# Kernel tuning notes

Hardware: AMD Instinct MI355X
Metric: run time of the kernel (lower is better)

## Reference

```python
import jax, jax.numpy as jnp
import numpy as np

B, C, HEADS, D, DKQ = 1024, 512, 8, 64, 8
DV = C // HEADS                 # 64, dim_head_v
QKVC = DV + 2 * DKQ             # 80, qkv channels per head
EPS = 1e-5


def _bn(x, g, b, m, v):
    # eval-mode batchnorm, channel axis = 1
    shp = (1, -1) + (1,) * (x.ndim - 2)
    scale = g.reshape(shp) / jnp.sqrt(v.reshape(shp) + EPS)
    return (x - m.reshape(shp)) * scale + b.reshape(shp)


def _rel_index():
    i = np.arange(D)
    # key_index - query_index + D - 1, row-major flatten -> (D*D,)
    return jnp.asarray((i[:, None] - i[None, :] + D - 1).reshape(-1))


def setup_inputs() -> dict:
    key = jax.random.key(0)
    ks = jax.random.split(key, 16)
    O = HEADS * QKVC
    d = {
        "x": jax.random.normal(ks[0], (B, C, D), jnp.float32),
        "conv_w": jax.random.normal(ks[1], (O, C), jnp.float32) * 0.02,
        "bn1_g": jax.random.normal(ks[2], (O,), jnp.float32) * 0.1 + 1.0,
        "bn1_b": jax.random.normal(ks[3], (O,), jnp.float32) * 0.1,
        "bn1_m": jax.random.normal(ks[4], (O,), jnp.float32) * 0.1,
        "bn1_v": jax.random.uniform(ks[5], (O,), jnp.float32) * 0.5 + 0.5,
        "rel": jax.random.normal(ks[6], (QKVC, 2 * D - 1), jnp.float32),
        "bn2_g": jax.random.normal(ks[7], (3 * HEADS,), jnp.float32) * 0.1 + 1.0,
        "bn2_b": jax.random.normal(ks[8], (3 * HEADS,), jnp.float32) * 0.1,
        "bn2_m": jax.random.normal(ks[9], (3 * HEADS,), jnp.float32) * 0.1,
        "bn2_v": jax.random.uniform(ks[10], (3 * HEADS,), jnp.float32) * 0.5 + 0.5,
        "bn3_g": jax.random.normal(ks[11], (2 * C,), jnp.float32) * 0.1 + 1.0,
        "bn3_b": jax.random.normal(ks[12], (2 * C,), jnp.float32) * 0.1,
        "bn3_m": jax.random.normal(ks[13], (2 * C,), jnp.float32) * 0.1,
        "bn3_v": jax.random.uniform(ks[14], (2 * C,), jnp.float32) * 0.5 + 0.5,
    }
    return d


def reference(x, conv_w, bn1_g, bn1_b, bn1_m, bn1_v, rel,
              bn2_g, bn2_b, bn2_m, bn2_v, bn3_g, bn3_b, bn3_m, bn3_v):
    # 1x1 conv1d + BN1d: [B, O, D]
    qkv = jnp.einsum('oc,bcd->bod', conv_w, x)
    qkv = _bn(qkv, bn1_g, bn1_b, bn1_m, bn1_v)
    # rearrange 'b (q h) d -> b h q d' with q=QKVC, h=HEADS (channel = q*H + h)
    qkv = qkv.reshape(B, QKVC, HEADS, D).transpose(0, 2, 1, 3)  # [B,H,QKVC,D]
    q = qkv[:, :, :DKQ]                # [B,H,DKQ,D]
    k = qkv[:, :, DKQ:2 * DKQ]         # [B,H,DKQ,D]
    v = qkv[:, :, 2 * DKQ:]            # [B,H,DV,D]

    # relative positional embeddings gathered from table
    emb = rel[:, _rel_index()].reshape(QKVC, D, D)
    r_q, r_k, r_v = emb[:DKQ], emb[DKQ:2 * DKQ], emb[2 * DKQ:]

    qr = jnp.einsum('bhid,idj->bhdj', q, r_q)
    kr = jnp.einsum('bhid,idj->bhdj', k, r_k)
    dots = jnp.einsum('bhid,bhij->bhdj', q, k)

    # rearrange 'n b h d j -> b (h n) d j'  (channel = h*3 + n)
    stacked = jnp.stack([qr, kr, dots], axis=2).reshape(B, 3 * HEADS, D, D)
    stacked = _bn(stacked, bn2_g, bn2_b, bn2_m, bn2_v)
    norm_dots = stacked.reshape(B, HEADS, 3, D, D).sum(axis=2)  # [B,H,D,D]

    attn = jax.nn.softmax(norm_dots, axis=-1)
    out = jnp.einsum('bhdj,bhij->bhid', attn, v)      # [B,H,DV,D]
    kv = jnp.einsum('bhdj,idj->bhid', attn, r_v)      # [B,H,DV,D]

    # rearrange 'n b h i d -> b (n h i) d'  (channel = n*H*DV + h*DV + i)
    st = jnp.stack([kv, out], axis=1).reshape(B, 2 * HEADS * DV, D)
    st = _bn(st, bn3_g, bn3_b, bn3_m, bn3_v)
    return st.reshape(B, 2, HEADS * DV, D).sum(axis=1)  # [B,C,D]
```

## Files before the change

### kernel.cpp

```cpp
#include <hip/hip_runtime.h>
#include <hip/hip_bf16.h>

#define B_    1024
#define C_    512
#define H_    8
#define D_    64
#define EPS_  1e-5f

typedef __attribute__((ext_vector_type(4))) float f32x4;
typedef __attribute__((ext_vector_type(8))) short bf16x8;
typedef __attribute__((ext_vector_type(8))) unsigned short u16x8;

__device__ __forceinline__ float bf2f(unsigned short h) {
    union { unsigned int u; float f; } c;
    c.u = ((unsigned int)h) << 16;
    return c.f;
}
__device__ __forceinline__ unsigned short f2bf(float f) {
    __hip_bfloat16 h = __float2bfloat16(f);
    return *reinterpret_cast<unsigned short*>(&h);
}

__global__ __launch_bounds__(256) void k0_wconv(
    const float* __restrict__ w, unsigned short* __restrict__ wf)
{
    int t = blockIdx.x * 256 + threadIdx.x;
    int o  = t >> 6;
    int c0 = (t & 63) * 8;
    const float* src = w + (size_t)o * C_ + c0;
    u16x8 p;
#pragma unroll
    for (int e = 0; e < 8; ++e) p[e] = f2bf(src[e]);
    int f = (o >> 4) * 16 + (c0 >> 5);
    int l = (o & 15) | (((c0 >> 3) & 3) << 4);
    *reinterpret_cast<u16x8*>(&wf[(size_t)f * 512 + l * 8]) = p;
}

__global__ __launch_bounds__(256) void k0_tables(
    const float* __restrict__ rel,
    const float* __restrict__ g2, const float* __restrict__ v2,
    const float* __restrict__ g3, const float* __restrict__ v3,
    unsigned short* __restrict__ relB, unsigned short* __restrict__ relvA)
{
    int tid = blockIdx.x * 256 + threadIdx.x;
    if (tid < 4096) {
        int h = tid >> 9, uf = (tid >> 6) & 7, l = tid & 63;
        int u = uf * 16 + (l & 15);
        int g = l >> 4;
        float sq = g2[3*h]     * rsqrtf(v2[3*h]     + EPS_);
        float sk = g2[3*h + 1] * rsqrtf(v2[3*h + 1] + EPS_);
        u16x8 p;
#pragma unroll
        for (int e = 0; e < 8; ++e) {
            int s = g * 8 + e;
            float val = 0.f;
            if (u < 127 && s < 16)
                val = (s < 8 ? sq : sk) * rel[s * 127 + u];
            p[e] = f2bf(val);
        }
        *reinterpret_cast<u16x8*>(&relB[(size_t)tid * 8]) = p;
    } else if (tid < 4096 + 8192) {
        int t2 = tid - 4096;
        int h = t2 >> 10, iF = (t2 >> 8) & 3, tt = (t2 >> 6) & 3, l = t2 & 63;
        int i = iF * 16 + (l & 15);
        int c3 = h * 64 + i;
        float scl = g3[c3] * rsqrtf(v3[c3] + EPS_);
        const float* rrow = rel + (size_t)(16 + i) * 127;
        u16x8 p;
#pragma unroll
        for (int e = 0; e < 8; ++e) {
            int u = (l >> 4) * 8 + e + 32 * tt;
            p[e] = f2bf((u < 127) ? scl * rrow[u] : 0.f);
        }
        *reinterpret_cast<u16x8*>(&relvA[(size_t)t2 * 8]) = p;
    }
}

#define LDW1 72

__global__ __launch_bounds__(512) void k1_gemm(
    const float* __restrict__ x, const unsigned short* __restrict__ wf,
    const float* __restrict__ g1, const float* __restrict__ b1,
    const float* __restrict__ m1, const float* __restrict__ v1,
    const float* __restrict__ g3, const float* __restrict__ v3,
    unsigned short* __restrict__ qkA, unsigned short* __restrict__ vB)
{
    __shared__ unsigned short xt[2][64 * LDW1];
    __shared__ float ssc[640], ssh[640];

    const int tid = threadIdx.x;
    const int b   = blockIdx.x;

    for (int t = tid; t < 640; t += 512) {
        float sc = g1[t] * rsqrtf(v1[t] + EPS_);
        float sh = b1[t] - m1[t] * sc;
        int cc = t >> 3, hh = t & 7;
        if (cc >= 16) {
            int c3 = 512 + hh * 64 + (cc - 16);
            float f = g3[c3] * rsqrtf(v3[c3] + EPS_);
            sc *= f; sh *= f;
        }
        ssc[t] = sc;
        ssh[t] = sh;
    }

    const int lane = tid & 63;
    const int wv   = tid >> 6;
    const int lm   = lane & 15;
    const int lg   = lane >> 4;

    const float* xb = x + (size_t)b * C_ * D_;
    const int cp = tid >> 4;
    const int c4 = (tid & 15) * 4;

    f32x4 acc[5][4];
#pragma unroll
    for (int i = 0; i < 5; ++i)
#pragma unroll
        for (int j = 0; j < 4; ++j) acc[i][j] = (f32x4){0.f, 0.f, 0.f, 0.f};

    {
        f32x4 a = *reinterpret_cast<const f32x4*>(&xb[(2 * cp) * 64 + c4]);
        f32x4 c = *reinterpret_cast<const f32x4*>(&xb[(2 * cp + 1) * 64 + c4]);
#pragma unroll
        for (int j = 0; j < 4; ++j) {
            unsigned int pk = (unsigned int)f2bf(a[j]) | ((unsigned int)f2bf(c[j]) << 16);
            *reinterpret_cast<unsigned int*>(&xt[0][(c4 + j) * LDW1 + 2 * cp]) = pk;
        }
    }
    __syncthreads();

    int cur = 0;
    for (int kt = 0; kt < 8; ++kt) {
        f32x4 pa, pc;
        if (kt < 7) {
            pa = *reinterpret_cast<const f32x4*>(&xb[((kt + 1) * 64 + 2 * cp) * 64 + c4]);
            pc = *reinterpret_cast<const f32x4*>(&xb[((kt + 1) * 64 + 2 * cp + 1) * 64 + c4]);
        }
#pragma unroll
        for (int ks = 0; ks < 2; ++ks) {
            bf16x8 af[5];
#pragma unroll
            for (int fm = 0; fm < 5; ++fm) {
                size_t f = (size_t)((wv * 5 + fm) * 16 + kt * 2 + ks) * 512;
                af[fm] = *reinterpret_cast<const bf16x8*>(&wf[f + lane * 8]);
            }
            bf16x8 bfr[4];
#pragma unroll
            for (int fn = 0; fn < 4; ++fn)
                bfr[fn] = *reinterpret_cast<const bf16x8*>(
                    &xt[cur][(fn * 16 + lm) * LDW1 + ks * 32 + lg * 8]);
#pragma unroll
            for (int fm = 0; fm < 5; ++fm)
#pragma unroll
                for (int fn = 0; fn < 4; ++fn)
                    acc[fm][fn] = __builtin_amdgcn_mfma_f32_16x16x32_bf16(
                        af[fm], bfr[fn], acc[fm][fn], 0, 0, 0);
        }
        if (kt < 7) {
#pragma unroll
            for (int j = 0; j < 4; ++j) {
                unsigned int pk = (unsigned int)f2bf(pa[j]) | ((unsigned int)f2bf(pc[j]) << 16);
                *reinterpret_cast<unsigned int*>(&xt[cur ^ 1][(c4 + j) * LDW1 + 2 * cp]) = pk;
            }
        }
        __syncthreads();
        cur ^= 1;
    }

#pragma unroll
    for (int fm = 0; fm < 5; ++fm) {
#pragma unroll
        for (int fn = 0; fn < 4; ++fn) {
            int d = fn * 16 + lm;
#pragma unroll
            for (int r = 0; r < 4; ++r) {
                int o = wv * 80 + fm * 16 + lg * 4 + r;
                int cc = o >> 3, hh = o & 7;
                float val = acc[fm][fn][r] * ssc[o] + ssh[o];
                unsigned short bv = f2bf(val);
                if (cc < 8)
                    qkA[(((size_t)b * 8 + hh) * 4 + (d >> 4)) * 512 + (d & 15) * 8 + cc] = bv;
                else if (cc < 16)
                    qkA[(((size_t)b * 8 + hh) * 4 + (d >> 4)) * 512 + ((d & 15) + 16) * 8 + (cc - 8)] = bv;
                else
                    vB[((size_t)(b * 8 + hh) * 64 + (cc - 16)) * 64 + d] = bv;
            }
        }
    }
    for (int z = tid; z < 4096; z += 512) {
        int hh  = z >> 9;
        int mf  = (z >> 7) & 3;
        int off = z & 127;
        unsigned int* p = reinterpret_cast<unsigned int*>(
            qkA + (((size_t)b * 8 + hh) * 4 + mf) * 512 + 256);
        p[off] = 0u;
    }
}

#define SGP 84
#define SA  72
#define RLD 136

__global__ __launch_bounds__(256) void k2_attn(
    const unsigned short* __restrict__ qkA, const unsigned short* __restrict__ vB,
    const unsigned short* __restrict__ relB, const unsigned short* __restrict__ relvA,
    const float* __restrict__ g2, const float* __restrict__ v2,
    const float* __restrict__ g3, const float* __restrict__ b3,
    const float* __restrict__ m3, const float* __restrict__ v3,
    float* __restrict__ outp)
{
    __shared__ float          SGb[64 * SGP];
    __shared__ unsigned short attn[64 * SA];
    __shared__ unsigned short A2[64 * RLD];
    __shared__ float sh3[64];

    const int tid  = threadIdx.x;
    const int b    = blockIdx.x >> 3;
    const int h    = blockIdx.x & 7;
    const int lane = tid & 63;
    const int w    = tid >> 6;
    const int lmm  = lane & 15;
    const int lg   = lane >> 4;

    const unsigned short* qbase = qkA + ((size_t)(b * 8 + h) * 4) * 512;

    for (int i = tid; i < 64 * RLD / 2; i += 256)
        reinterpret_cast<unsigned int*>(A2)[i] = 0u;
    if (tid < 64) {
        int c = h * 64 + tid;
        float sa = g3[c] * rsqrtf(v3[c] + EPS_);
        float sb = g3[512 + c] * rsqrtf(v3[512 + c] + EPS_);
        sh3[tid] = (b3[c] - m3[c] * sa) + (b3[512 + c] - m3[512 + c] * sb);
    }
    const float s_dt = g2[3 * h + 2] * rsqrtf(v2[3 * h + 2] + EPS_);

    bf16x8 aA = *reinterpret_cast<const bf16x8*>(&qbase[w * 512 + lane * 8]);
    bf16x8 zv = {0, 0, 0, 0, 0, 0, 0, 0};
    bf16x8 kBf[4];
#pragma unroll
    for (int jf = 0; jf < 4; ++jf) {
        kBf[jf] = zv;
        if (lane < 16)
            kBf[jf] = *reinterpret_cast<const bf16x8*>(&qbase[jf * 512 + (lane + 16) * 8]);
    }
    bf16x8 rBf[8];
#pragma unroll
    for (int uf = 0; uf < 8; ++uf)
        rBf[uf] = *reinterpret_cast<const bf16x8*>(&relB[(size_t)(h * 8 + uf) * 512 + lane * 8]);

    f32x4 dotsAcc[4];
#pragma unroll
    for (int jf = 0; jf < 4; ++jf)
        dotsAcc[jf] = __builtin_amdgcn_mfma_f32_16x16x32_bf16(
            aA, kBf[jf], (f32x4){0.f, 0.f, 0.f, 0.f}, 0, 0, 0);
    f32x4 sgAcc[8];
#pragma unroll
    for (int uf = 0; uf < 8; ++uf)
        sgAcc[uf] = __builtin_amdgcn_mfma_f32_16x16x32_bf16(
            aA, rBf[uf], (f32x4){0.f, 0.f, 0.f, 0.f}, 0, 0, 0);

#pragma unroll
    for (int uf = 0; uf < 8; ++uf) {
#pragma unroll
        for (int r = 0; r < 4; ++r) {
            int d = (w << 4) + (lg << 2) + r;
            int t = uf * 16 + lmm - d + 15;
            if (t >= 0 && t < 79)
                SGb[d * SGP + t] = sgAcc[uf][r];
        }
    }
    __syncthreads();

#pragma unroll
    for (int r = 0; r < 4; ++r) {
        int d = (w << 4) + (lg << 2) + r;
        const float* sgr = &SGb[d * SGP];
        float sc0 = s_dt * dotsAcc[0][r] + sgr[78 - lmm];
        float sc1 = s_dt * dotsAcc[1][r] + sgr[62 - lmm];
        float sc2 = s_dt * dotsAcc[2][r] + sgr[46 - lmm];
        float sc3 = s_dt * dotsAcc[3][r] + sgr[30 - lmm];
        float mx = fmaxf(fmaxf(sc0, sc1), fmaxf(sc2, sc3));
        mx = fmaxf(mx, __shfl_xor(mx, 1));
        mx = fmaxf(mx, __shfl_xor(mx, 2));
        mx = fmaxf(mx, __shfl_xor(mx, 4));
        mx = fmaxf(mx, __shfl_xor(mx, 8));
        float e0 = __expf(sc0 - mx), e1 = __expf(sc1 - mx);
        float e2 = __expf(sc2 - mx), e3 = __expf(sc3 - mx);
        float sum = (e0 + e1) + (e2 + e3);
        sum += __shfl_xor(sum, 1);
        sum += __shfl_xor(sum, 2);
        sum += __shfl_xor(sum, 4);
        sum += __shfl_xor(sum, 8);
        float inv = 1.f / sum;
        unsigned short p0 = f2bf(e0 * inv), p1 = f2bf(e1 * inv);
        unsigned short p2 = f2bf(e2 * inv), p3 = f2bf(e3 * inv);
        attn[d * SA + lmm]      = p0;
        attn[d * SA + 16 + lmm] = p1;
        attn[d * SA + 32 + lmm] = p2;
        attn[d * SA + 48 + lmm] = p3;
        A2[d * RLD + 63 + d - lmm] = p0;
        A2[d * RLD + 47 + d - lmm] = p1;
        A2[d * RLD + 31 + d - lmm] = p2;
        A2[d * RLD + 15 + d - lmm] = p3;
    }

    const int lk8  = lg * 8;
    const int irow = (w << 4) + lmm;
    const unsigned short* vbase = vB + (size_t)(b * 8 + h) * 4096;
    bf16x8 av0 = *reinterpret_cast<const bf16x8*>(&vbase[irow * 64 + lk8]);
    bf16x8 av1 = *reinterpret_cast<const bf16x8*>(&vbase[irow * 64 + 32 + lk8]);
    bf16x8 rvA[4];
#pragma unroll
    for (int t = 0; t < 4; ++t)
        rvA[t] = *reinterpret_cast<const bf16x8*>(
            &relvA[(size_t)(((h * 4 + w) * 4 + t)) * 512 + lane * 8]);

    __syncthreads();

    f32x4 acc[4];
#pragma unroll
    for (int nf = 0; nf < 4; ++nf) acc[nf] = (f32x4){0.f, 0.f, 0.f, 0.f};

#pragma unroll
    for (int nf = 0; nf < 4; ++nf) {
        const unsigned short* arow = &attn[(nf * 16 + lmm) * SA + lk8];
        acc[nf] = __builtin_amdgcn_mfma_f32_16x16x32_bf16(
            av0, *reinterpret_cast<const bf16x8*>(&arow[0]), acc[nf], 0, 0, 0);
        acc[nf] = __builtin_amdgcn_mfma_f32_16x16x32_bf16(
            av1, *reinterpret_cast<const bf16x8*>(&arow[32]), acc[nf], 0, 0, 0);
        const unsigned short* a2row = &A2[(nf * 16 + lmm) * RLD + lk8];
        acc[nf] = __builtin_amdgcn_mfma_f32_16x16x32_bf16(
            rvA[0], *reinterpret_cast<const bf16x8*>(&a2row[0]), acc[nf], 0, 0, 0);
        acc[nf] = __builtin_amdgcn_mfma_f32_16x16x32_bf16(
            rvA[1], *reinterpret_cast<const bf16x8*>(&a2row[32]), acc[nf], 0, 0, 0);
        acc[nf] = __builtin_amdgcn_mfma_f32_16x16x32_bf16(
            rvA[2], *reinterpret_cast<const bf16x8*>(&a2row[64]), acc[nf], 0, 0, 0);
        acc[nf] = __builtin_amdgcn_mfma_f32_16x16x32_bf16(
            rvA[3], *reinterpret_cast<const bf16x8*>(&a2row[96]), acc[nf], 0, 0, 0);
    }

    float* op = outp + ((size_t)b * 512 + h * 64) * 64;
    const int r0 = lg * 4;
#pragma unroll
    for (int r = 0; r < 4; ++r) {
        int i = (w << 4) + r0 + r;
        float sh = sh3[i];
#pragma unroll
        for (int nf = 0; nf < 4; ++nf)
            op[(size_t)i * 64 + nf * 16 + lmm] = acc[nf][r] + sh;
    }
}

extern "C" void kernel_launch(void* const* d_in, const int* in_sizes, int n_in,
                              void* d_out, int out_size, void* d_ws, size_t ws_size,
                              hipStream_t stream) {
    (void)in_sizes; (void)n_in; (void)out_size; (void)ws_size;
    const float* x   = (const float*)d_in[0];
    const float* w   = (const float*)d_in[1];
    const float* g1  = (const float*)d_in[2];
    const float* b1  = (const float*)d_in[3];
    const float* m1  = (const float*)d_in[4];
    const float* v1  = (const float*)d_in[5];
    const float* rel = (const float*)d_in[6];
    const float* g2  = (const float*)d_in[7];
    const float* b2  = (const float*)d_in[8];  (void)b2;
    const float* m2  = (const float*)d_in[9];  (void)m2;
    const float* v2  = (const float*)d_in[10];
    const float* g3  = (const float*)d_in[11];
    const float* b3  = (const float*)d_in[12];
    const float* m3  = (const float*)d_in[13];
    const float* v3  = (const float*)d_in[14];
    float* out = (float*)d_out;

    unsigned short* wfrag = (unsigned short*)d_ws;
    unsigned short* relB  = (unsigned short*)((char*)d_ws + 655360);
    unsigned short* relvA = (unsigned short*)((char*)d_ws + 720896);
    unsigned short* qkA   = (unsigned short*)((char*)d_ws + 1048576);
    unsigned short* vB    = (unsigned short*)((char*)d_ws + 1048576 + (size_t)33554432);

    hipLaunchKernelGGL(k0_wconv, dim3(160), dim3(256), 0, stream, w, wfrag);
    hipLaunchKernelGGL(k0_tables, dim3(48), dim3(256), 0, stream,
                       rel, g2, v2, g3, v3, relB, relvA);
    hipLaunchKernelGGL(k1_gemm, dim3(1024), dim3(512), 0, stream,
                       x, wfrag, g1, b1, m1, v1, g3, v3, qkA, vB);
    hipLaunchKernelGGL(k2_attn, dim3(8192), dim3(256), 0, stream,
                       qkA, vB, relB, relvA, g2, v2, g3, b3, m3, v3, out);
}
```

Before: 192.1 us.

## Stage whole x tile into fragment-ordered LDS once instead of double-buffered k-loop

The QKV projection GEMM now loads the full 512x64 x slice for a batch element into shared memory in one up-front pass. It stores it in MFMA B-fragment order, so each lane reads a contiguous 16-byte vector with no padding. The previous double-buffered loop, with a barrier per k-tile, is replaced by a fully unrolled 16-step MFMA loop with no intermediate syncs. A launch-bounds occupancy hint is also added. The costs are 64KB of LDS per block, which limits blocks per CU, and no overlap between the global loads and the MFMAs.

New measurement: 207.8 us. 8.2% more time.

```diff
diff --git a/kernel.cpp b/kernel.cpp
--- a/kernel.cpp
+++ b/kernel.cpp
@@ -76,16 +76,14 @@
     }
 }
 
-#define LDW1 72
-
-__global__ __launch_bounds__(512) void k1_gemm(
+__global__ __launch_bounds__(512, 4) void k1_gemm(
     const float* __restrict__ x, const unsigned short* __restrict__ wf,
     const float* __restrict__ g1, const float* __restrict__ b1,
     const float* __restrict__ m1, const float* __restrict__ v1,
     const float* __restrict__ g3, const float* __restrict__ v3,
     unsigned short* __restrict__ qkA, unsigned short* __restrict__ vB)
 {
-    __shared__ unsigned short xt[2][64 * LDW1];
+    __shared__ unsigned short xf[16 * 4 * 64 * 8];
     __shared__ float ssc[640], ssh[640];
 
     const int tid = threadIdx.x;
@@ -104,68 +102,60 @@
         ssh[t] = sh;
     }
 
+    const float* xb = x + (size_t)b * C_ * D_;
+#pragma unroll
+    for (int it = 0; it < 2; ++it) {
+        int t  = tid + it * 512;
+        int c0 = (t >> 4) * 8;
+        int d0 = (t & 15) * 4;
+        f32x4 row[8];
+#pragma unroll
+        for (int cc = 0; cc < 8; ++cc)
+            row[cc] = *reinterpret_cast<const f32x4*>(&xb[(c0 + cc) * 64 + d0]);
+        int ks = c0 >> 5;
+        int kg = (c0 >> 3) & 3;
+#pragma unroll
+        for (int dd = 0; dd < 4; ++dd) {
+            int d  = d0 + dd;
+            int fn = d >> 4;
+            int ln = (d & 15) | (kg << 4);
+            u16x8 p;
+#pragma unroll
+            for (int e = 0; e < 8; ++e) p[e] = f2bf(row[e][dd]);
+            *reinterpret_cast<u16x8*>(&xf[((ks * 4 + fn) * 64 + ln) * 8]) = p;
+        }
+    }
+    __syncthreads();
+
     const int lane = tid & 63;
     const int wv   = tid >> 6;
     const int lm   = lane & 15;
     const int lg   = lane >> 4;
 
-    const float* xb = x + (size_t)b * C_ * D_;
-    const int cp = tid >> 4;
-    const int c4 = (tid & 15) * 4;
-
     f32x4 acc[5][4];
 #pragma unroll
     for (int i = 0; i < 5; ++i)
 #pragma unroll
         for (int j = 0; j < 4; ++j) acc[i][j] = (f32x4){0.f, 0.f, 0.f, 0.f};
 
-    {
-        f32x4 a = *reinterpret_cast<const f32x4*>(&xb[(2 * cp) * 64 + c4]);
-        f32x4 c = *reinterpret_cast<const f32x4*>(&xb[(2 * cp + 1) * 64 + c4]);
-#pragma unroll
-        for (int j = 0; j < 4; ++j) {
-            unsigned int pk = (unsigned int)f2bf(a[j]) | ((unsigned int)f2bf(c[j]) << 16);
-            *reinterpret_cast<unsigned int*>(&xt[0][(c4 + j) * LDW1 + 2 * cp]) = pk;
-        }
-    }
-    __syncthreads();
-
-    int cur = 0;
-    for (int kt = 0; kt < 8; ++kt) {
-        f32x4 pa, pc;
-        if (kt < 7) {
-            pa = *reinterpret_cast<const f32x4*>(&xb[((kt + 1) * 64 + 2 * cp) * 64 + c4]);
-            pc = *reinterpret_cast<const f32x4*>(&xb[((kt + 1) * 64 + 2 * cp + 1) * 64 + c4]);
-        }
-#pragma unroll
-        for (int ks = 0; ks < 2; ++ks) {
-            bf16x8 af[5];
-#pragma unroll
-            for (int fm = 0; fm < 5; ++fm) {
-                size_t f = (size_t)((wv * 5 + fm) * 16 + kt * 2 + ks) * 512;
-                af[fm] = *reinterpret_cast<const bf16x8*>(&wf[f + lane * 8]);
-            }
-            bf16x8 bfr[4];
+    const unsigned short* wfw = wf + (size_t)(wv * 5) * 16 * 512 + lane * 8;
+    const unsigned short* xfl = xf + lane * 8;
+
+#pragma unroll
+    for (int ks = 0; ks < 16; ++ks) {
+        bf16x8 af[5], bfr[4];
+#pragma unroll
+        for (int fm = 0; fm < 5; ++fm)
+            af[fm] = *reinterpret_cast<const bf16x8*>(&wfw[(size_t)(fm * 16 + ks) * 512]);
+#pragma unroll
+        for (int fn = 0; fn < 4; ++fn)
+            bfr[fn] = *reinterpret_cast<const bf16x8*>(&xfl[(ks * 4 + fn) * 512]);
+#pragma unroll
+        for (int fm = 0; fm < 5; ++fm)
 #pragma unroll
             for (int fn = 0; fn < 4; ++fn)
-                bfr[fn] = *reinterpret_cast<const bf16x8*>(
-                    &xt[cur][(fn * 16 + lm) * LDW1 + ks * 32 + lg * 8]);
-#pragma unroll
-            for (int fm = 0; fm < 5; ++fm)
-#pragma unroll
-                for (int fn = 0; fn < 4; ++fn)
-                    acc[fm][fn] = __builtin_amdgcn_mfma_f32_16x16x32_bf16(
-                        af[fm], bfr[fn], acc[fm][fn], 0, 0, 0);
-        }
-        if (kt < 7) {
-#pragma unroll
-            for (int j = 0; j < 4; ++j) {
-                unsigned int pk = (unsigned int)f2bf(pa[j]) | ((unsigned int)f2bf(pc[j]) << 16);
-                *reinterpret_cast<unsigned int*>(&xt[cur ^ 1][(c4 + j) * LDW1 + 2 * cp]) = pk;
-            }
-        }
-        __syncthreads();
-        cur ^= 1;
+                acc[fm][fn] = __builtin_amdgcn_mfma_f32_16x16x32_bf16(
+                    af[fm], bfr[fn], acc[fm][fn], 0, 0, 0);
     }
 
 #pragma unroll
```
